# Kernel optimization log

Hardware: AMD Instinct MI355X
Metric: run time of the kernel (lower is better)

The kernel has to match this reference:

```python
import jax, jax.numpy as jnp
import numpy as np

B, S, IN = 8, 1024, 64
D, F, H, L = 512, 2048, 8, 6
HD = D // H
EPS = 1e-5
GATE_TEMP = 1.0


def _rmsnorm(x, scale):
    return x * scale * jax.lax.rsqrt(jnp.mean(x * x, axis=-1, keepdims=True) + EPS)


def _sinusoidal_pe(seq_len, d_model):
    pos = np.arange(seq_len)[:, None].astype(np.float32)
    div = np.exp(np.arange(0, d_model, 2).astype(np.float32) * (-np.log(10000.0) / d_model))
    pe = np.zeros((seq_len, d_model), dtype=np.float32)
    pe[:, 0::2] = np.sin(pos * div)
    pe[:, 1::2] = np.cos(pos * div)
    return jnp.asarray(pe)


def setup_inputs() -> dict:
    key = jax.random.key(0)
    ks = jax.random.split(key, 12)
    s = 0.02
    return {
        "src": jax.random.normal(ks[0], (B, S, IN), jnp.float32),
        "in_w": jax.random.normal(ks[1], (IN, D), jnp.float32) * s,
        "in_b": jnp.zeros((D,), jnp.float32),
        "Wq": jax.random.normal(ks[2], (L, D, D), jnp.float32) * s,
        "Wk": jax.random.normal(ks[3], (L, D, D), jnp.float32) * s,
        "Wv": jax.random.normal(ks[4], (L, D, D), jnp.float32) * s,
        "Wo": jax.random.normal(ks[5], (L, D, D), jnp.float32) * s,
        "bq": jnp.zeros((L, D), jnp.float32),
        "bk": jnp.zeros((L, D), jnp.float32),
        "bv": jnp.zeros((L, D), jnp.float32),
        "bo": jnp.zeros((L, D), jnp.float32),
        "n1": jnp.ones((L, D), jnp.float32),
        "n2": jnp.ones((L, D), jnp.float32),
        "Wg": jax.random.normal(ks[6], (L, D, F), jnp.float32) * s,
        "Wu": jax.random.normal(ks[7], (L, D, F), jnp.float32) * s,
        "Wd": jax.random.normal(ks[8], (L, F, D), jnp.float32) * s,
        "gate_w": jax.random.normal(ks[9], (L, D), jnp.float32) * s,
        "gate_b": jnp.full((L,), 2.0, jnp.float32),  # LayerGate init_bias=2.0
        "final_scale": jnp.ones((D,), jnp.float32),
    }


def reference(src, in_w, in_b, Wq, Wk, Wv, Wo, bq, bk, bv, bo, n1, n2,
              Wg, Wu, Wd, gate_w, gate_b, final_scale):
    b, s, _ = src.shape
    x = src @ in_w + in_b                      # input_adapter: [B,S,D]
    x = x + _sinusoidal_pe(s, D)               # PositionalEncoding, scale=1.0
    inv_sqrt_hd = 1.0 / jnp.sqrt(jnp.asarray(HD, x.dtype))
    for i in range(L):
        # --- pre-norm self-attention block ---
        h = _rmsnorm(x, n1[i])
        q = (h @ Wq[i] + bq[i]).reshape(b, s, H, HD)
        k = (h @ Wk[i] + bk[i]).reshape(b, s, H, HD)
        v = (h @ Wv[i] + bv[i]).reshape(b, s, H, HD)
        scores = jnp.einsum("bqhd,bkhd->bhqk", q, k) * inv_sqrt_hd
        attn = jax.nn.softmax(scores, axis=-1)
        ctx = jnp.einsum("bhqk,bkhd->bqhd", attn, v).reshape(b, s, D)
        y = x + (ctx @ Wo[i] + bo[i])
        # --- pre-norm SwiGLU FFN block ---
        h2 = _rmsnorm(y, n2[i])
        y = y + (jax.nn.silu(h2 @ Wg[i]) * (h2 @ Wu[i])) @ Wd[i]
        # --- LayerGate: seq-mode hard skip with straight-through estimator ---
        pooled = jnp.mean(x, axis=1)                           # gate on layer input [B,D]
        p = jax.nn.sigmoid((pooled @ gate_w[i] + gate_b[i]) / GATE_TEMP)  # [B]
        hard = (p > 0.5).astype(x.dtype)
        g = hard + p - jax.lax.stop_gradient(p)
        x = g[:, None, None] * y + (1.0 - g)[:, None, None] * x
    return _rmsnorm(x, final_scale)
```

## Files before the change

kernel.cpp:

```cpp
#include <hip/hip_runtime.h>


typedef unsigned short u16;
typedef __attribute__((ext_vector_type(8))) __bf16 bf16x8;
typedef __attribute__((ext_vector_type(4))) float f32x4;
typedef __attribute__((ext_vector_type(16))) float f32x16;
typedef __attribute__((ext_vector_type(8))) unsigned short u16x8;

#define DEV __device__ __forceinline__

DEV u16 f2bf(float f) {
  unsigned u = __builtin_bit_cast(unsigned, f);
  u += 0x7fffu + ((u >> 16) & 1u);
  return (u16)(u >> 16);
}
DEV float bf2f(u16 h) { return __builtin_bit_cast(float, ((unsigned)h) << 16); }

DEV void gload16(const void* g, void* l) {
  __builtin_amdgcn_global_load_lds(
      (__attribute__((address_space(1))) void*)g,
      (__attribute__((address_space(3))) void*)l, 16, 0, 0);
}

DEV void xcd_map(int& bx, int& by) {
  const int nx = gridDim.x, ny = gridDim.y;
  const int orig = by * nx + bx;
  const int cpx = (nx * ny) >> 3;
  const int swz = (orig & 7) * cpx + (orig >> 3);
  by = swz / nx; bx = swz - by * nx;
}

DEV void xcd_map2d_byout(int& bx, int& by) {
  const int nx = gridDim.x, ny = gridDim.y;
  const int orig = by * nx + bx;
  const int xcd = orig & 7, rnk = orig >> 3;
  const int hx = nx >> 1, qy = ny >> 2;
  bx = (xcd & 1) * hx + rnk % hx;
  by = (xcd >> 1) * qy + rnk / hx;
}

__global__ __launch_bounds__(256) void transpose_all_kernel(
    const float* __restrict__ Wq, const float* __restrict__ Wk,
    const float* __restrict__ Wv, const float* __restrict__ Wo,
    const float* __restrict__ Wg, const float* __restrict__ Wu,
    const float* __restrict__ Wd,
    u16* __restrict__ WqkvT, u16* __restrict__ WoT, u16* __restrict__ WgT,
    u16* __restrict__ WuT, u16* __restrict__ WdT)
{
  const int l = blockIdx.y;
  const int idx = blockIdx.x;
  const float* src; u16* dst; int N, bx, by;
  if (idx < 1024) {
    const int w = idx >> 8, t = idx & 255;
    bx = t & 15; by = t >> 4; N = 512;
    const size_t lo = (size_t)l * 262144;
    if (w == 0)      { src = Wq + lo; dst = WqkvT + (size_t)l * 786432; }
    else if (w == 1) { src = Wk + lo; dst = WqkvT + (size_t)l * 786432 + 262144; }
    else if (w == 2) { src = Wv + lo; dst = WqkvT + (size_t)l * 786432 + 524288; }
    else             { src = Wo + lo; dst = WoT + lo; }
  } else if (idx < 2048) {
    const int t = idx - 1024; bx = t & 63; by = t >> 6; N = 2048;
    src = Wg + (size_t)l * 1048576; dst = WgT + (size_t)l * 1048576;
  } else if (idx < 3072) {
    const int t = idx - 2048; bx = t & 63; by = t >> 6; N = 2048;
    src = Wu + (size_t)l * 1048576; dst = WuT + (size_t)l * 1048576;
  } else {
    const int t = idx - 3072; bx = t & 15; by = t >> 4; N = 512;
    src = Wd + (size_t)l * 1048576; dst = WdT + (size_t)l * 1048576;
  }
  const int K = (idx >= 3072) ? 2048 : 512;
  __shared__ float tl[32][33];
  const int n0 = bx * 32, k0 = by * 32;
  const int tx = threadIdx.x & 31, ty = threadIdx.x >> 5;
#pragma unroll
  for (int i = 0; i < 4; ++i)
    tl[ty + i * 8][tx] = src[(size_t)(k0 + ty + i * 8) * N + n0 + tx];
  __syncthreads();
#pragma unroll
  for (int i = 0; i < 4; ++i)
    dst[(size_t)(n0 + ty + i * 8) * K + k0 + tx] = f2bf(tl[tx][ty + i * 8]);
}

__global__ void biaspack_kernel(const float* __restrict__ bq,
                                const float* __restrict__ bk,
                                const float* __restrict__ bv,
                                float* __restrict__ out)
{
  const int l = blockIdx.x;
  for (int c = threadIdx.x; c < 1536; c += 256) {
    float v = (c < 512) ? bq[l * 512 + c]
            : (c < 1024) ? bk[l * 512 + c - 512]
                         : bv[l * 512 + c - 1024];
    out[l * 1536 + c] = v;
  }
}

__global__ __launch_bounds__(256) void adapter_kernel(
    const float* __restrict__ src, const float* __restrict__ w,
    const float* __restrict__ bias, float* __restrict__ x)
{
  __shared__ float srow[8][64];
  const int m0 = blockIdx.y * 8;
  const int n = blockIdx.x * 256 + threadIdx.x;
  for (int i = threadIdx.x; i < 512; i += 256)
    srow[i >> 6][i & 63] = src[(size_t)m0 * 64 + i];
  __syncthreads();
  float acc[8];
#pragma unroll
  for (int r = 0; r < 8; ++r) acc[r] = bias[n];
  for (int k = 0; k < 64; ++k) {
    const float wv = w[(size_t)k * 512 + n];
#pragma unroll
    for (int r = 0; r < 8; ++r) acc[r] = fmaf(srow[r][k], wv, acc[r]);
  }
  const int i2 = n & ~1;
  const float freq = expf((float)i2 * (-9.210340371976184f / 512.0f));
#pragma unroll
  for (int r = 0; r < 8; ++r) {
    const int pos = (m0 + r) & 1023;
    const float ang = (float)pos * freq;
    acc[r] += (n & 1) ? cosf(ang) : sinf(ang);
    x[(size_t)(m0 + r) * 512 + n] = acc[r];
  }
}

template <bool BF16OUT, bool GATE>
__global__ __launch_bounds__(256) void rmsnorm_kernel(
    const float* __restrict__ x, const float* __restrict__ scale,
    u16* __restrict__ outb, float* __restrict__ outf,
    const float* __restrict__ gw, float* __restrict__ gp2)
{
  const int wave = threadIdx.x >> 6, lane = threadIdx.x & 63;
  const size_t row = (size_t)blockIdx.x * 4 + wave;
  const f32x4* xr = (const f32x4*)(x + row * 512);
  f32x4 a = xr[lane * 2], c = xr[lane * 2 + 1];
  float ss = a[0]*a[0] + a[1]*a[1] + a[2]*a[2] + a[3]*a[3]
           + c[0]*c[0] + c[1]*c[1] + c[2]*c[2] + c[3]*c[3];
  float dv = 0.0f;
  if (GATE) {
    const f32x4* gr = (const f32x4*)gw;
    f32x4 g1 = gr[lane * 2], g2 = gr[lane * 2 + 1];
    dv = a[0]*g1[0] + a[1]*g1[1] + a[2]*g1[2] + a[3]*g1[3]
       + c[0]*g2[0] + c[1]*g2[1] + c[2]*g2[2] + c[3]*g2[3];
  }
#pragma unroll
  for (int d = 1; d < 64; d <<= 1) {
    ss += __shfl_xor(ss, d);
    if (GATE) dv += __shfl_xor(dv, d);
  }
  if (GATE && lane == 0) gp2[blockIdx.x * 4 + wave] = dv;
  const float r = rsqrtf(ss * (1.0f / 512.0f) + 1e-5f);
  const f32x4* sr = (const f32x4*)scale;
  f32x4 s1 = sr[lane * 2], s2 = sr[lane * 2 + 1];
  if (BF16OUT) {
    u16x8 ov;
    ov[0] = f2bf(a[0] * s1[0] * r); ov[1] = f2bf(a[1] * s1[1] * r);
    ov[2] = f2bf(a[2] * s1[2] * r); ov[3] = f2bf(a[3] * s1[3] * r);
    ov[4] = f2bf(c[0] * s2[0] * r); ov[5] = f2bf(c[1] * s2[1] * r);
    ov[6] = f2bf(c[2] * s2[2] * r); ov[7] = f2bf(c[3] * s2[3] * r);
    *(u16x8*)(outb + row * 512 + lane * 8) = ov;
  } else {
    f32x4 o1, o2;
    o1[0] = a[0]*s1[0]*r; o1[1] = a[1]*s1[1]*r; o1[2] = a[2]*s1[2]*r; o1[3] = a[3]*s1[3]*r;
    o2[0] = c[0]*s2[0]*r; o2[1] = c[1]*s2[1]*r; o2[2] = c[2]*s2[2]*r; o2[3] = c[3]*s2[3]*r;
    f32x4* orow = (f32x4*)(outf + row * 512);
    orow[lane * 2] = o1; orow[lane * 2 + 1] = o2;
  }
}

template <int MODE, int BN, int MAP>
__global__ __launch_bounds__(256) void gemm_bt(
    const u16* __restrict__ A, const u16* __restrict__ Bt,
    const float* __restrict__ bias, const float* __restrict__ resf,
    float* __restrict__ outf, u16* __restrict__ outb,
    const float* __restrict__ gatep, const float* __restrict__ gbias,
    int layer, int M, int N, int K)
{
  constexpr int NI = BN / 32;
  __shared__ __align__(16) u16 lA[128 * 64];
  __shared__ __align__(16) u16 lB[BN * 64];
  const int tid = threadIdx.x;
  const int wave = tid >> 6, lane = tid & 63;
  const int lr = lane & 15, lg = lane >> 4;
  int bx = blockIdx.x, by = blockIdx.y;
  if (MAP == 0) xcd_map(bx, by); else xcd_map2d_byout(bx, by);
  const int m0 = by << 7, n0 = bx * BN;
  const int wr = wave >> 1, wc = wave & 1;
  if (MODE == 4) {
    __shared__ float red[64];
    __shared__ float gfl;
    const float* g4 = gatep + (size_t)(m0 >> 10) * 256;
    float v = (tid < 256) ? g4[tid] : 0.0f;
#pragma unroll
    for (int d = 1; d < 64; d <<= 1) v += __shfl_xor(v, d);
    if (lane == 0) red[wave] = v;
    __syncthreads();
    if (tid == 0) {
      const float s = red[0] + red[1] + red[2] + red[3];
      gfl = (s / 1024.0f + gbias[layer] > 0.0f) ? 1.0f : 0.0f;
    }
    __syncthreads();
    if (gfl == 0.0f) return;
  }
  f32x4 acc[4][NI] = {};
  for (int kt = 0; kt < K; kt += 64) {
    __syncthreads();
#pragma unroll
    for (int i = 0; i < 4; ++i) {
      const int c = i * 256 + tid;
      const int row = c >> 3, kc = ((c & 7) ^ (row & 7)) << 3;
      gload16(A + (size_t)(m0 + row) * K + kt + kc,
              lA + (size_t)(i * 256 + wave * 64) * 8);
    }
#pragma unroll
    for (int i = 0; i < BN / 32; ++i) {
      const int c = i * 256 + tid;
      const int row = c >> 3, kc = ((c & 7) ^ (row & 7)) << 3;
      gload16(Bt + (size_t)(n0 + row) * K + kt + kc,
              lB + (size_t)(i * 256 + wave * 64) * 8);
    }
    __syncthreads();
    bf16x8 af[2][4], bfr[2][NI];
#pragma unroll
    for (int kk = 0; kk < 2; ++kk) {
#pragma unroll
      for (int mi = 0; mi < 4; ++mi) {
        const int row = wr * 64 + mi * 16 + lr;
        af[kk][mi] = *(const bf16x8*)&lA[row * 64 + (((kk * 4 + lg) ^ (row & 7)) << 3)];
      }
#pragma unroll
      for (int ni = 0; ni < NI; ++ni) {
        const int row = wc * (BN / 2) + ni * 16 + lr;
        bfr[kk][ni] = *(const bf16x8*)&lB[row * 64 + (((kk * 4 + lg) ^ (row & 7)) << 3)];
      }
    }
#pragma unroll
    for (int kk = 0; kk < 2; ++kk)
#pragma unroll
      for (int mi = 0; mi < 4; ++mi)
#pragma unroll
        for (int ni = 0; ni < NI; ++ni)
          acc[mi][ni] = __builtin_amdgcn_mfma_f32_16x16x32_bf16(
              af[kk][mi], bfr[kk][ni], acc[mi][ni], 0, 0, 0);
  }
#pragma unroll
  for (int mi = 0; mi < 4; ++mi) {
#pragma unroll
    for (int ni = 0; ni < NI; ++ni) {
      const int col = n0 + wc * (BN / 2) + ni * 16 + lr;
      const float bs = (MODE == 0 || MODE == 1) ? bias[col] : 0.0f;
#pragma unroll
      for (int j = 0; j < 4; ++j) {
        const int row = m0 + wr * 64 + mi * 16 + lg * 4 + j;
        const size_t idx = (size_t)row * N + col;
        float v = acc[mi][ni][j] + bs;
        if (MODE == 0) {
          if (col < 512) v *= 0.125f;
          outb[idx] = f2bf(v);
        } else {
          outf[idx] = v + resf[idx];
        }
      }
    }
  }
}

__global__ __launch_bounds__(256) void gemm_glu(
    const u16* __restrict__ A, const u16* __restrict__ Bg,
    const u16* __restrict__ Bu, u16* __restrict__ outT)
{
  constexpr int K = 512, N = 2048;
  __shared__ __align__(16) u16 lA[128 * 64];
  __shared__ __align__(16) u16 lG[64 * 64];
  __shared__ __align__(16) u16 lU[64 * 64];
  const int tid = threadIdx.x;
  const int wave = tid >> 6, lane = tid & 63;
  const int lr = lane & 15, lg = lane >> 4;
  const int orig = blockIdx.y * gridDim.x + blockIdx.x;
  const int xcd = orig & 7, rnk = orig >> 3;
  const int bx = (xcd & 1) * 16 + (rnk >> 4);
  const int by = (xcd >> 1) * 16 + (rnk & 15);
  const int m0 = by << 7, n0 = bx << 6;
  const int wr = wave >> 1, wc = wave & 1;
  f32x4 ag[4][2] = {}, au[4][2] = {};
  for (int kt = 0; kt < K; kt += 64) {
    __syncthreads();
#pragma unroll
    for (int i = 0; i < 4; ++i) {
      const int c = i * 256 + tid;
      const int row = c >> 3, kc = ((c & 7) ^ (row & 7)) << 3;
      gload16(A + (size_t)(m0 + row) * K + kt + kc,
              lA + (size_t)(i * 256 + wave * 64) * 8);
    }
#pragma unroll
    for (int i = 0; i < 2; ++i) {
      const int c = i * 256 + tid;
      const int row = c >> 3, kc = ((c & 7) ^ (row & 7)) << 3;
      const size_t dst = (size_t)(i * 256 + wave * 64) * 8;
      gload16(Bg + (size_t)(n0 + row) * K + kt + kc, lG + dst);
      gload16(Bu + (size_t)(n0 + row) * K + kt + kc, lU + dst);
    }
    __syncthreads();
    bf16x8 af[2][4], gf[2][2], uf[2][2];
#pragma unroll
    for (int kk = 0; kk < 2; ++kk) {
#pragma unroll
      for (int mi = 0; mi < 4; ++mi) {
        const int row = wr * 64 + mi * 16 + lr;
        af[kk][mi] = *(const bf16x8*)&lA[row * 64 + (((kk * 4 + lg) ^ (row & 7)) << 3)];
      }
#pragma unroll
      for (int ni = 0; ni < 2; ++ni) {
        const int row = wc * 32 + ni * 16 + lr;
        const int off = row * 64 + (((kk * 4 + lg) ^ (row & 7)) << 3);
        gf[kk][ni] = *(const bf16x8*)&lG[off];
        uf[kk][ni] = *(const bf16x8*)&lU[off];
      }
    }
#pragma unroll
    for (int kk = 0; kk < 2; ++kk)
#pragma unroll
      for (int mi = 0; mi < 4; ++mi)
#pragma unroll
        for (int ni = 0; ni < 2; ++ni) {
          ag[mi][ni] = __builtin_amdgcn_mfma_f32_16x16x32_bf16(
              af[kk][mi], gf[kk][ni], ag[mi][ni], 0, 0, 0);
          au[mi][ni] = __builtin_amdgcn_mfma_f32_16x16x32_bf16(
              af[kk][mi], uf[kk][ni], au[mi][ni], 0, 0, 0);
        }
  }
#pragma unroll
  for (int mi = 0; mi < 4; ++mi) {
#pragma unroll
    for (int ni = 0; ni < 2; ++ni) {
      const int col = n0 + wc * 32 + ni * 16 + lr;
#pragma unroll
      for (int j = 0; j < 4; ++j) {
        const int row = m0 + wr * 64 + mi * 16 + lg * 4 + j;
        const float g = ag[mi][ni][j];
        const float sg = g / (1.0f + __expf(-g));
        outT[(size_t)row * N + col] = f2bf(sg * au[mi][ni][j]);
      }
    }
  }
}

__global__ __launch_bounds__(256) void attn_kernel(
    const u16* __restrict__ qkv, u16* __restrict__ ctx)
{
  constexpr int LD = 1536;
  const int qblk = blockIdx.x, bh = blockIdx.y;
  const int b = bh >> 3, h = bh & 7;
  const int tid = threadIdx.x, wave = tid >> 6, lane = tid & 63;
  const int l31 = lane & 31, half = lane >> 5;
  const size_t rowb = (size_t)b * 1024;
  const int q0 = qblk * 128 + wave * 32;

  __shared__ __align__(16) u16 Ksh[2][64 * 64];
  __shared__ __align__(16) u16 Vsh[2][64 * 72];
  __shared__ __align__(16) u16 PL[4][32 * 64];
  __shared__ float rl_lds[4][32];

  const u16* qrow = qkv + (rowb + q0 + l31) * LD + h * 64;
  bf16x8 qf[4];
#pragma unroll
  for (int c = 0; c < 4; ++c)
    qf[c] = *(const bf16x8*)(qrow + c * 16 + half * 8);

  const int krow0 = tid >> 3;
  const int kch0 = (tid & 7) ^ (krow0 & 7);
  const int vm = tid >> 3, vd0 = (tid & 7) * 8;
  const int vcol = ((vm >> 2) << 4) + ((vm & 3) << 2);
  char* vbase0 = (char*)Vsh[0] + vcol;
  const u16* kg = qkv + rowb * LD + 512 + h * 64;
  const u16* vg = qkv + (rowb + 2 * vm) * LD + 1024 + h * 64 + vd0;

  f32x16 o0 = {}, o1 = {};
  float l_acc = 0.0f;

  gload16(kg + (size_t)(0 + krow0) * LD + kch0 * 8, Ksh[0] + wave * 512);
  gload16(kg + (size_t)(32 + krow0) * LD + kch0 * 8, Ksh[0] + 2048 + wave * 512);
  {
    u16x8 va = *(const u16x8*)vg;
    u16x8 vb = *(const u16x8*)(vg + LD);
#pragma unroll
    for (int j = 0; j < 8; ++j) {
      const unsigned w = (unsigned)va[j] | ((unsigned)vb[j] << 16);
      *(unsigned*)(vbase0 + (vd0 + j) * 144) = w;
    }
  }
  __syncthreads();

  for (int t = 0; t < 16; ++t) {
    const int cur = t & 1, nxt = cur ^ 1;
    const int k0n = (t + 1) * 64;
    u16x8 va2, vb2;
    if (t < 15) {
      gload16(kg + (size_t)(k0n + krow0) * LD + kch0 * 8,
              Ksh[nxt] + wave * 512);
      gload16(kg + (size_t)(k0n + 32 + krow0) * LD + kch0 * 8,
              Ksh[nxt] + 2048 + wave * 512);
      va2 = *(const u16x8*)(vg + (size_t)k0n * LD);
      vb2 = *(const u16x8*)(vg + (size_t)k0n * LD + LD);
    }

    const char* kshb = (const char*)Ksh[cur];
    const char* vshb = (const char*)Vsh[cur];

    f32x16 s0 = {}, s1 = {};
#pragma unroll
    for (int c = 0; c < 4; ++c) {
      {
        const int row = l31;
        bf16x8 kf = *(const bf16x8*)(kshb + row * 128 +
                        ((((c << 1) | half) ^ (row & 7)) << 4));
        s0 = __builtin_amdgcn_mfma_f32_32x32x16_bf16(kf, qf[c], s0, 0, 0, 0);
      }
      {
        const int row = 32 + l31;
        bf16x8 kf = *(const bf16x8*)(kshb + row * 128 +
                        ((((c << 1) | half) ^ (row & 7)) << 4));
        s1 = __builtin_amdgcn_mfma_f32_32x32x16_bf16(kf, qf[c], s1, 0, 0, 0);
      }
    }

    char* plw = (char*)PL[wave];
#pragma unroll
    for (int blk = 0; blk < 2; ++blk) {
      const f32x16 sv = blk ? s1 : s0;
#pragma unroll
      for (int rg = 0; rg < 4; ++rg) {
        const float e0 = __expf(fminf(sv[rg * 4 + 0], 60.0f));
        const float e1 = __expf(fminf(sv[rg * 4 + 1], 60.0f));
        const float e2 = __expf(fminf(sv[rg * 4 + 2], 60.0f));
        const float e3 = __expf(fminf(sv[rg * 4 + 3], 60.0f));
        l_acc += (e0 + e1) + (e2 + e3);
        const unsigned lo = (unsigned)f2bf(e0) | ((unsigned)f2bf(e1) << 16);
        const unsigned hi = (unsigned)f2bf(e2) | ((unsigned)f2bf(e3) << 16);
        const int chunk = (rg + 4 * blk) ^ (l31 & 7);
        *(unsigned long long*)(plw + l31 * 128 + (chunk << 4) + half * 8) =
            (unsigned long long)lo | ((unsigned long long)hi << 32);
      }
    }

#pragma unroll
    for (int c = 0; c < 4; ++c) {
      bf16x8 pf = *(const bf16x8*)(plw + l31 * 128 +
                      ((((c << 1) | half) ^ (l31 & 7)) << 4));
      {
        const int row = l31;
        bf16x8 vf = *(const bf16x8*)(vshb + row * 144 +
                        (((c << 1) | half) << 4));
        o0 = __builtin_amdgcn_mfma_f32_32x32x16_bf16(pf, vf, o0, 0, 0, 0);
      }
      {
        const int row = 32 + l31;
        bf16x8 vf = *(const bf16x8*)(vshb + row * 144 +
                        (((c << 1) | half) << 4));
        o1 = __builtin_amdgcn_mfma_f32_32x32x16_bf16(pf, vf, o1, 0, 0, 0);
      }
    }

    if (t < 15) {
      char* vbn = (char*)Vsh[nxt] + vcol;
#pragma unroll
      for (int j = 0; j < 8; ++j) {
        const unsigned w = (unsigned)va2[j] | ((unsigned)vb2[j] << 16);
        *(unsigned*)(vbn + (vd0 + j) * 144) = w;
      }
    }
    __syncthreads();
  }

  const float l_tot = l_acc + __shfl_xor(l_acc, 32);
  if (lane < 32) rl_lds[wave][l31] = 1.0f / l_tot;
  __syncthreads();
#pragma unroll
  for (int r = 0; r < 16; ++r) {
    const int q_r = (r & 3) + 8 * (r >> 2) + 4 * half;
    const float rl = rl_lds[wave][q_r];
    const size_t orow = (rowb + q0 + q_r) * 512 + h * 64 + l31;
    ctx[orow] = f2bf(o0[r] * rl);
    ctx[orow + 32] = f2bf(o1[r] * rl);
  }
}

extern "C" void kernel_launch(void* const* d_in, const int* in_sizes, int n_in,
                              void* d_out, int out_size, void* d_ws, size_t ws_size,
                              hipStream_t stream)
{
  (void)in_sizes; (void)n_in; (void)out_size; (void)ws_size;
  const float* src  = (const float*)d_in[0];
  const float* in_w = (const float*)d_in[1];
  const float* in_b = (const float*)d_in[2];
  const float* Wq   = (const float*)d_in[3];
  const float* Wk   = (const float*)d_in[4];
  const float* Wv   = (const float*)d_in[5];
  const float* Wo   = (const float*)d_in[6];
  const float* bq   = (const float*)d_in[7];
  const float* bk   = (const float*)d_in[8];
  const float* bv   = (const float*)d_in[9];
  const float* bo   = (const float*)d_in[10];
  const float* n1   = (const float*)d_in[11];
  const float* n2   = (const float*)d_in[12];
  const float* Wg   = (const float*)d_in[13];
  const float* Wu   = (const float*)d_in[14];
  const float* Wd   = (const float*)d_in[15];
  const float* gw   = (const float*)d_in[16];
  const float* gb   = (const float*)d_in[17];
  const float* fs   = (const float*)d_in[18];

  char* ws = (char*)d_ws;
  size_t off = 0;
  auto alloc = [&](size_t bytes) -> void* {
    void* p = ws + off;
    off += (bytes + 255) & ~(size_t)255;
    return p;
  };
  u16*   WqkvT = (u16*)alloc(6ULL * 1536 * 512 * 2);
  u16*   WoT   = (u16*)alloc(6ULL * 512 * 512 * 2);
  u16*   WgT   = (u16*)alloc(6ULL * 2048 * 512 * 2);
  u16*   WuT   = (u16*)alloc(6ULL * 2048 * 512 * 2);
  u16*   WdT   = (u16*)alloc(6ULL * 512 * 2048 * 2);
  float* bqkv  = (float*)alloc(6ULL * 1536 * 4);
  float* x     = (float*)alloc(8192ULL * 512 * 4);
  float* y     = (float*)alloc(8192ULL * 512 * 4);
  u16*   hbuf  = (u16*)alloc(8192ULL * 512 * 2);
  u16*   sA    = (u16*)alloc(8192ULL * 2048 * 2);
  u16*   sB    = (u16*)alloc(8192ULL * 2048 * 2);
  float* gp2   = (float*)alloc(8192 * 4);

  const dim3 tb(256);
  transpose_all_kernel<<<dim3(4096, 6), tb, 0, stream>>>(
      Wq, Wk, Wv, Wo, Wg, Wu, Wd, WqkvT, WoT, WgT, WuT, WdT);
  biaspack_kernel<<<6, tb, 0, stream>>>(bq, bk, bv, bqkv);
  adapter_kernel<<<dim3(2, 1024), tb, 0, stream>>>(src, in_w, in_b, x);

  for (int l = 0; l < 6; ++l) {
    rmsnorm_kernel<true, true><<<2048, tb, 0, stream>>>(
        x, n1 + l * 512, hbuf, nullptr, gw + l * 512, gp2);
    gemm_bt<0, 128, 0><<<dim3(12, 64), tb, 0, stream>>>(
        hbuf, WqkvT + (size_t)l * 1536 * 512, bqkv + l * 1536,
        nullptr, nullptr, sA, nullptr, nullptr, 0, 8192, 1536, 512);
    attn_kernel<<<dim3(8, 64), tb, 0, stream>>>(sA, sB);
    gemm_bt<1, 64, 0><<<dim3(8, 64), tb, 0, stream>>>(
        sB, WoT + (size_t)l * 512 * 512, bo + l * 512,
        x, y, nullptr, nullptr, nullptr, 0, 8192, 512, 512);
    rmsnorm_kernel<true, false><<<2048, tb, 0, stream>>>(
        y, n2 + l * 512, hbuf, nullptr, nullptr, nullptr);
    gemm_glu<<<dim3(32, 64), tb, 0, stream>>>(
        hbuf, WgT + (size_t)l * 2048 * 512, WuT + (size_t)l * 2048 * 512, sB);
    gemm_bt<4, 64, 1><<<dim3(8, 64), tb, 0, stream>>>(
        sB, WdT + (size_t)l * 512 * 2048, nullptr,
        y, x, nullptr, gp2, gb, l, 8192, 512, 2048);
  }
  rmsnorm_kernel<false, false><<<2048, tb, 0, stream>>>(
      x, fs, nullptr, (float*)d_out, nullptr, nullptr);
}
```

Baseline: 988.5 us.

## Rewrite SwiGLU GEMM with 8-wave 256-row tiles and triple-buffered LDS pipeline

The gate/up GEMM moves to 512-thread blocks that each cover 256 rows by 64 columns, so every loaded weight tile feeds twice as many rows. It uses a three-stage LDS ring, issuing async global-to-LDS loads two k-steps ahead and waiting with explicit vmcnt counts instead of a full sync before and after every step. The down-projection GEMM goes back to the plain XCD swizzle and the 2D by-output mapping is deleted. LDS use per block grows to about 144 KB, which limits residency to one block per CU and depends on the hand-written waitcnt counts being correct.

```diff
diff --git a/kernel.cpp b/kernel.cpp
--- a/kernel.cpp
+++ b/kernel.cpp
@@ -28,15 +28,6 @@
   const int cpx = (nx * ny) >> 3;
   const int swz = (orig & 7) * cpx + (orig >> 3);
   by = swz / nx; bx = swz - by * nx;
-}
-
-DEV void xcd_map2d_byout(int& bx, int& by) {
-  const int nx = gridDim.x, ny = gridDim.y;
-  const int orig = by * nx + bx;
-  const int xcd = orig & 7, rnk = orig >> 3;
-  const int hx = nx >> 1, qy = ny >> 2;
-  bx = (xcd & 1) * hx + rnk % hx;
-  by = (xcd >> 1) * qy + rnk / hx;
 }
 
 __global__ __launch_bounds__(256) void transpose_all_kernel(
@@ -168,7 +159,7 @@
   }
 }
 
-template <int MODE, int BN, int MAP>
+template <int MODE, int BN>
 __global__ __launch_bounds__(256) void gemm_bt(
     const u16* __restrict__ A, const u16* __restrict__ Bt,
     const float* __restrict__ bias, const float* __restrict__ resf,
@@ -183,7 +174,7 @@
   const int wave = tid >> 6, lane = tid & 63;
   const int lr = lane & 15, lg = lane >> 4;
   int bx = blockIdx.x, by = blockIdx.y;
-  if (MAP == 0) xcd_map(bx, by); else xcd_map2d_byout(bx, by);
+  xcd_map(bx, by);
   const int m0 = by << 7, n0 = bx * BN;
   const int wr = wave >> 1, wc = wave & 1;
   if (MODE == 4) {
@@ -265,56 +256,67 @@
   }
 }
 
-__global__ __launch_bounds__(256) void gemm_glu(
+__global__ __launch_bounds__(512) void gemm_glu8(
     const u16* __restrict__ A, const u16* __restrict__ Bg,
     const u16* __restrict__ Bu, u16* __restrict__ outT)
 {
-  constexpr int K = 512, N = 2048;
-  __shared__ __align__(16) u16 lA[128 * 64];
-  __shared__ __align__(16) u16 lG[64 * 64];
-  __shared__ __align__(16) u16 lU[64 * 64];
+  constexpr int K = 512, N = 2048, NK = K / 64;
+  __shared__ __align__(16) u16 lA[3][256 * 64];
+  __shared__ __align__(16) u16 lG[3][64 * 64];
+  __shared__ __align__(16) u16 lU[3][64 * 64];
   const int tid = threadIdx.x;
   const int wave = tid >> 6, lane = tid & 63;
   const int lr = lane & 15, lg = lane >> 4;
-  const int orig = blockIdx.y * gridDim.x + blockIdx.x;
+  const int orig = blockIdx.y * 32 + blockIdx.x;
   const int xcd = orig & 7, rnk = orig >> 3;
-  const int bx = (xcd & 1) * 16 + (rnk >> 4);
-  const int by = (xcd >> 1) * 16 + (rnk & 15);
-  const int m0 = by << 7, n0 = bx << 6;
+  const int bx = (xcd & 1) * 16 + (rnk >> 3);
+  const int by = (xcd >> 1) * 8 + (rnk & 7);
+  const int m0 = by << 8, n0 = bx << 6;
   const int wr = wave >> 1, wc = wave & 1;
-  f32x4 ag[4][2] = {}, au[4][2] = {};
-  for (int kt = 0; kt < K; kt += 64) {
-    __syncthreads();
+
+  auto stage = [&](int buf, int kt) {
 #pragma unroll
     for (int i = 0; i < 4; ++i) {
-      const int c = i * 256 + tid;
+      const int c = i * 512 + tid;
       const int row = c >> 3, kc = ((c & 7) ^ (row & 7)) << 3;
       gload16(A + (size_t)(m0 + row) * K + kt + kc,
-              lA + (size_t)(i * 256 + wave * 64) * 8);
-    }
-#pragma unroll
-    for (int i = 0; i < 2; ++i) {
-      const int c = i * 256 + tid;
-      const int row = c >> 3, kc = ((c & 7) ^ (row & 7)) << 3;
-      const size_t dst = (size_t)(i * 256 + wave * 64) * 8;
-      gload16(Bg + (size_t)(n0 + row) * K + kt + kc, lG + dst);
-      gload16(Bu + (size_t)(n0 + row) * K + kt + kc, lU + dst);
-    }
-    __syncthreads();
+              lA[buf] + (size_t)(i * 512 + wave * 64) * 8);
+    }
+    {
+      const int row = tid >> 3, kc = ((tid & 7) ^ (row & 7)) << 3;
+      gload16(Bg + (size_t)(n0 + row) * K + kt + kc,
+              lG[buf] + (size_t)(wave * 64) * 8);
+      gload16(Bu + (size_t)(n0 + row) * K + kt + kc,
+              lU[buf] + (size_t)(wave * 64) * 8);
+    }
+  };
+
+  f32x4 ag[4][2] = {}, au[4][2] = {};
+  stage(0, 0);
+  stage(1, 64);
+  asm volatile("s_waitcnt vmcnt(6)" ::: "memory");
+  __builtin_amdgcn_s_barrier();
+
+#pragma unroll
+  for (int t = 0; t < NK; ++t) {
+    if (t + 2 < NK) stage((t + 2) % 3, (t + 2) * 64);
+    const u16* la = lA[t % 3];
+    const u16* lgb = lG[t % 3];
+    const u16* lub = lU[t % 3];
     bf16x8 af[2][4], gf[2][2], uf[2][2];
 #pragma unroll
     for (int kk = 0; kk < 2; ++kk) {
 #pragma unroll
       for (int mi = 0; mi < 4; ++mi) {
         const int row = wr * 64 + mi * 16 + lr;
-        af[kk][mi] = *(const bf16x8*)&lA[row * 64 + (((kk * 4 + lg) ^ (row & 7)) << 3)];
+        af[kk][mi] = *(const bf16x8*)&la[row * 64 + (((kk * 4 + lg) ^ (row & 7)) << 3)];
       }
 #pragma unroll
       for (int ni = 0; ni < 2; ++ni) {
         const int row = wc * 32 + ni * 16 + lr;
         const int off = row * 64 + (((kk * 4 + lg) ^ (row & 7)) << 3);
-        gf[kk][ni] = *(const bf16x8*)&lG[off];
-        uf[kk][ni] = *(const bf16x8*)&lU[off];
+        gf[kk][ni] = *(const bf16x8*)&lgb[off];
+        uf[kk][ni] = *(const bf16x8*)&lub[off];
       }
     }
 #pragma unroll
@@ -328,7 +330,14 @@
           au[mi][ni] = __builtin_amdgcn_mfma_f32_16x16x32_bf16(
               af[kk][mi], uf[kk][ni], au[mi][ni], 0, 0, 0);
         }
-  }
+    if (t + 2 < NK) {
+      asm volatile("s_waitcnt vmcnt(6)" ::: "memory");
+    } else if (t + 1 < NK) {
+      asm volatile("s_waitcnt vmcnt(0)" ::: "memory");
+    }
+    __builtin_amdgcn_s_barrier();
+  }
+
 #pragma unroll
   for (int mi = 0; mi < 4; ++mi) {
 #pragma unroll
@@ -539,18 +548,18 @@
   for (int l = 0; l < 6; ++l) {
     rmsnorm_kernel<true, true><<<2048, tb, 0, stream>>>(
         x, n1 + l * 512, hbuf, nullptr, gw + l * 512, gp2);
-    gemm_bt<0, 128, 0><<<dim3(12, 64), tb, 0, stream>>>(
+    gemm_bt<0, 128><<<dim3(12, 64), tb, 0, stream>>>(
         hbuf, WqkvT + (size_t)l * 1536 * 512, bqkv + l * 1536,
         nullptr, nullptr, sA, nullptr, nullptr, 0, 8192, 1536, 512);
     attn_kernel<<<dim3(8, 64), tb, 0, stream>>>(sA, sB);
-    gemm_bt<1, 64, 0><<<dim3(8, 64), tb, 0, stream>>>(
+    gemm_bt<1, 64><<<dim3(8, 64), tb, 0, stream>>>(
         sB, WoT + (size_t)l * 512 * 512, bo + l * 512,
         x, y, nullptr, nullptr, nullptr, 0, 8192, 512, 512);
     rmsnorm_kernel<true, false><<<2048, tb, 0, stream>>>(
         y, n2 + l * 512, hbuf, nullptr, nullptr, nullptr);
-    gemm_glu<<<dim3(32, 64), tb, 0, stream>>>(
+    gemm_glu8<<<dim3(32, 32), dim3(512), 0, stream>>>(
         hbuf, WgT + (size_t)l * 2048 * 512, WuT + (size_t)l * 2048 * 512, sB);
-    gemm_bt<4, 64, 1><<<dim3(8, 64), tb, 0, stream>>>(
+    gemm_bt<4, 64><<<dim3(8, 64), tb, 0, stream>>>(
         sB, WdT + (size_t)l * 512 * 2048, nullptr,
         y, x, nullptr, gp2, gb, l, 8192, 512, 2048);
   }
```

Measured after the change: 1.032 ms. +4.4%, slower.
